# Kernel optimization log

Measured on AMD Instinct MI355X. Metric: run time of the kernel, lower is better.

Reference implementation:

```python
import jax, jax.numpy as jnp
import numpy as np

DIM = 3
N_GRID = 128
DX = 1.0 / N_GRID
INV_DX = float(N_GRID)
DT = 1e-4
P_VOL = (DX * 0.5) ** 2
P_RHO = 1.0
P_MASS = P_VOL * P_RHO
E_MOD = 5000.0
NU = 0.2
MU0 = E_MOD / (2.0 * (1.0 + NU))
LAM0 = E_MOD * NU / ((1.0 + NU) * (1.0 - 2.0 * NU))
N_PARTICLES = 400_000

# 27 stencil offsets of the quadratic B-spline kernel
_OFF = jnp.array([[i, j, k] for i in range(3) for j in range(3) for k in range(3)],
                 dtype=jnp.int32)  # [27,3]


def _substep(x, v, C, F, Jp, gravity, attractor_strength, attractor_pos, material):
    N = x.shape[0]
    dtype = x.dtype
    I3 = jnp.eye(3, dtype=dtype)

    # ---- particle -> grid (P2G) ----
    base = jnp.floor(x * INV_DX - 0.5).astype(jnp.int32)          # [N,3]
    fx = x * INV_DX - base.astype(dtype)                          # [N,3]
    # quadratic kernel weights, w[a, n, d], a in {0,1,2}
    w = jnp.stack([0.5 * (1.5 - fx) ** 2,
                   0.75 - (fx - 1.0) ** 2,
                   0.5 * (fx - 0.5) ** 2], axis=0)                # [3,N,3]

    Fn = jnp.einsum('nij,njk->nik', I3 + DT * C, F)               # deformation update

    h = jnp.clip(jnp.exp(10.0 * (1.0 - Jp)), 0.1, 5.0)
    h = jnp.where(material == 1, 0.3, h)
    mu = jnp.where(material == 0, 0.0, MU0 * h)                   # [N]
    la = LAM0 * h                                                 # [N]

    U, s, Vh = jnp.linalg.svd(Fn, full_matrices=False)            # [N,3,3],[N,3],[N,3,3]

    # faithful to source: plasticity loop only touches first TWO singular values
    J = jnp.ones_like(Jp)
    sig = s
    for d in range(2):
        new_sig = jnp.where(material == 2,
                            jnp.clip(s[:, d], 1.0 - 0.025, 1.0 + 0.0045),
                            s[:, d])
        Jp = Jp * s[:, d] / new_sig
        sig = sig.at[:, d].set(new_sig)
        J = J * new_sig

    F_fluid = jnp.sqrt(J)[:, None, None] * I3                     # material 0
    F_snow = jnpum = None
    F_snow = jnp.einsum('nij,nj,njk->nik', U, sig, Vh)            # material 2: U diag(sig) V^T
    m3 = material[:, None, None]
    Fn = jnp.where(m3 == 0, F_fluid, jnp.where(m3 == 2, F_snow, Fn))

    R = jnp.einsum('nij,njk->nik', U, Vh)                         # U V^T (rotation)
    stress = (2.0 * mu[:, None, None] * jnp.einsum('nij,nkj->nik', Fn - R, Fn)
              + I3 * (la * J * (J - 1.0))[:, None, None])
    stress = (-DT * P_VOL * 4.0 * INV_DX * INV_DX) * stress
    affine = stress + P_MASS * C                                  # [N,3,3]

    # NOTE faithful quirk of the source: weight = w[i][0] * w[j][1] (k-component unused)
    weight = w[_OFF[:, 0], :, 0] * w[_OFF[:, 1], :, 1]            # [27,N]
    dpos = (_OFF[:, None, :].astype(dtype) - fx[None]) * DX       # [27,N,3]
    mom = weight[..., None] * (P_MASS * v[None]
                               + jnp.einsum('nij,onj->oni', affine, dpos))  # [27,N,3]

    idx = base[None] + _OFF[:, None, :]                           # [27,N,3]
    flat = (idx[..., 0] * N_GRID + idx[..., 1]) * N_GRID + idx[..., 2]      # [27,N]
    G3 = N_GRID ** 3
    grid_mom = jnp.zeros((G3, 3), dtype).at[flat.reshape(-1)].add(mom.reshape(-1, 3))
    grid_m = jnp.zeros((G3,), dtype).at[flat.reshape(-1)].add((weight * P_MASS).reshape(-1))

    # ---- grid update ----
    a = jnp.arange(N_GRID, dtype=jnp.int32)
    coords = jnp.stack(jnp.meshgrid(a, a, a, indexing='ij'), axis=-1).reshape(G3, 3)
    mask = grid_m > 0
    m_safe = jnp.where(mask, grid_m, 1.0)
    gv = grid_mom / m_safe[:, None]
    gv = gv + DT * gravity * 30.0
    dist = attractor_pos[None, :] - DX * coords.astype(dtype)
    gv = gv + dist / (0.01 + jnp.linalg.norm(dist, axis=-1, keepdims=True)) \
              * attractor_strength * DT * 100.0
    ic, jc = coords[:, 0], coords[:, 1]
    vx, vy, vz = gv[:, 0], gv[:, 1], gv[:, 2]
    vx = jnp.where((ic < 3) & (vx < 0), 0.0, vx)
    vx = jnp.where((ic > N_GRID - 3) & (vx > 0), 0.0, vx)
    vy = jnp.where((jc < 3) & (vy < 0), 0.0, vy)
    vy = jnp.where((jc > N_GRID - 3) & (vy > 0), 0.0, vy)
    gv = jnp.stack([vx, vy, vz], axis=-1)
    gv = jnp.where(mask[:, None], gv, 0.0)                        # untouched cells stay zero

    # ---- grid -> particle (G2P) ----
    g_v = gv[flat]                                                # [27,N,3]
    dpos2 = _OFF[:, None, :].astype(dtype) - fx[None]             # [27,N,3] (no dx scale)
    new_v = jnp.einsum('on,onc->nc', weight, g_v)                 # [N,3]
    new_C = 4.0 * INV_DX * jnp.einsum('on,onc,ond->ncd', weight, g_v, dpos2)  # [N,3,3]
    x_new = x + DT * new_v

    # pack state: [x(3) | v(3) | Jp(1) | F(9) | C(9)] -> [N,25]
    return jnp.concatenate([x_new, new_v, Jp[:, None],
                            Fn.reshape(N, 9), new_C.reshape(N, 9)], axis=1)


def setup_inputs() -> dict:
    key = jax.random.key(0)
    ks = jax.random.split(key, 9)
    N = N_PARTICLES
    x = 0.1 + 0.8 * jax.random.uniform(ks[0], (N, 3), dtype=jnp.float32)
    v = 0.1 * jax.random.normal(ks[1], (N, 3), dtype=jnp.float32)
    C = 0.01 * jax.random.normal(ks[2], (N, 3, 3), dtype=jnp.float32)
    F = jnp.eye(3, dtype=jnp.float32) + 0.01 * jax.random.normal(ks[3], (N, 3, 3), dtype=jnp.float32)
    Jp = 1.0 + 0.1 * jax.random.uniform(ks[4], (N,), dtype=jnp.float32)
    material = jax.random.randint(ks[5], (N,), 0, 3, dtype=jnp.int32)
    gravity = jnp.array([0.0, -1.0, 0.0], dtype=jnp.float32)
    attractor_strength = jax.random.uniform(ks[6], (), dtype=jnp.float32)
    attractor_pos = jax.random.uniform(ks[7], (3,), dtype=jnp.float32)
    return {"x": x, "v": v, "C": C, "F": F, "Jp": Jp,
            "gravity": gravity, "attractor_strength": attractor_strength,
            "attractor_pos": attractor_pos, "material": material}


def reference(x, v, C, F, Jp, gravity, attractor_strength, attractor_pos, material):
    return _substep(x, v, C, F, Jp, gravity, attractor_strength, attractor_pos, material)
```

## Files before the change

kernel.cpp:

```cpp
#include <hip/hip_runtime.h>

#define NG 128
#define G3 (NG*NG*NG)
#define NSCAN_BLOCKS (G3/256)

__device__ __constant__ const float c_DX      = 1.0f/128.0f;
__device__ __constant__ const float c_INV_DX  = 128.0f;

#define DT      1e-4f
#define P_VOL   ((1.0f/256.0f)*(1.0f/256.0f))
#define P_MASS  P_VOL
#define MU0     (5000.0f/(2.0f*1.2f))
#define LAM0    (5000.0f*0.2f/(1.2f*0.6f))

struct __align__(16) PRec {
    float4 r0, r1, r2, r3;
};

__device__ inline void jacobi_rot(float S[3][3], float V[3][3], int p, int q) {
    float apq = S[p][q];
    if (fabsf(apq) < 1e-24f) return;
    float tau = (S[q][q] - S[p][p]) / (2.0f * apq);
    float t = copysignf(1.0f, tau) / (fabsf(tau) + sqrtf(1.0f + tau*tau));
    float c = rsqrtf(1.0f + t*t);
    float sn = t * c;
    #pragma unroll
    for (int k = 0; k < 3; ++k) {
        float Spk = S[p][k], Sqk = S[q][k];
        S[p][k] = c*Spk - sn*Sqk;
        S[q][k] = sn*Spk + c*Sqk;
    }
    #pragma unroll
    for (int k = 0; k < 3; ++k) {
        float Skp = S[k][p], Skq = S[k][q];
        S[k][p] = c*Skp - sn*Skq;
        S[k][q] = sn*Skp + c*Skq;
    }
    #pragma unroll
    for (int k = 0; k < 3; ++k) {
        float Vkp = V[k][p], Vkq = V[k][q];
        V[k][p] = c*Vkp - sn*Vkq;
        V[k][q] = sn*Vkp + c*Vkq;
    }
}

__device__ inline void svd3(const float A[9], float U[9], float sv[3], float V[9]) {
    float S[3][3];
    #pragma unroll
    for (int i = 0; i < 3; ++i)
        #pragma unroll
        for (int j = 0; j < 3; ++j) {
            float acc = 0.f;
            #pragma unroll
            for (int k = 0; k < 3; ++k) acc += A[k*3+i]*A[k*3+j];
            S[i][j] = acc;
        }
    float Vm[3][3] = {{1.f,0.f,0.f},{0.f,1.f,0.f},{0.f,0.f,1.f}};
    #pragma unroll
    for (int sweep = 0; sweep < 4; ++sweep) {
        jacobi_rot(S, Vm, 0, 1);
        jacobi_rot(S, Vm, 0, 2);
        jacobi_rot(S, Vm, 1, 2);
    }
    float lam[3] = {S[0][0], S[1][1], S[2][2]};
    int i0 = 0, i1 = 1, i2 = 2, t;
    if (lam[i0] < lam[i1]) { t = i0; i0 = i1; i1 = t; }
    if (lam[i0] < lam[i2]) { t = i0; i0 = i2; i2 = t; }
    if (lam[i1] < lam[i2]) { t = i1; i1 = i2; i2 = t; }
    int ord[3] = {i0, i1, i2};
    #pragma unroll
    for (int c = 0; c < 3; ++c) {
        int s_ = ord[c];
        float l = fmaxf(lam[s_], 0.f);
        float sval = sqrtf(l);
        sv[c] = sval;
        float v0 = Vm[0][s_], v1 = Vm[1][s_], v2 = Vm[2][s_];
        V[0*3+c] = v0; V[1*3+c] = v1; V[2*3+c] = v2;
        float inv = (sval > 1e-12f) ? 1.0f/sval : 0.f;
        U[0*3+c] = (A[0]*v0 + A[1]*v1 + A[2]*v2)*inv;
        U[1*3+c] = (A[3]*v0 + A[4]*v1 + A[5]*v2)*inv;
        U[2*3+c] = (A[6]*v0 + A[7]*v1 + A[8]*v2)*inv;
    }
}

__device__ inline void base_from_A(float A0, float A1, float A2,
                                   int& bi, int& bj, int& bk,
                                   float& fx0, float& fx1, float& fx2) {
    float bxf = floorf(A0 - 0.5f);
    float byf = floorf(A1 - 0.5f);
    float bzf = floorf(A2 - 0.5f);
    bi = (int)bxf; bj = (int)byf; bk = (int)bzf;
    bi = min(max(bi, 0), NG-3); bj = min(max(bj, 0), NG-3); bk = min(max(bk, 0), NG-3);
    fx0 = A0 - bxf;
    fx1 = A1 - byf;
    fx2 = A2 - bzf;
}

__global__ void __launch_bounds__(256)
count_kernel(const float* __restrict__ x, int* __restrict__ cell_count, int N) {
    int n = blockIdx.x*256 + threadIdx.x;
    if (n >= N) return;
    int bi, bj, bk; float f0, f1, f2;
    base_from_A(x[3*n+0]*c_INV_DX, x[3*n+1]*c_INV_DX, x[3*n+2]*c_INV_DX,
                bi, bj, bk, f0, f1, f2);
    atomicAdd(&cell_count[(bi*NG + bj)*NG + bk], 1);
}

__global__ void __launch_bounds__(256)
scan_partial_kernel(const int* __restrict__ count, int* __restrict__ partial) {
    __shared__ int red[256];
    int t = threadIdx.x;
    red[t] = count[blockIdx.x*256 + t];
    __syncthreads();
    for (int off = 128; off > 0; off >>= 1) {
        if (t < off) red[t] += red[t+off];
        __syncthreads();
    }
    if (t == 0) partial[blockIdx.x] = red[0];
}

__global__ void __launch_bounds__(256)
scan_partials_kernel(int* __restrict__ partial) {
    __shared__ int part[256];
    int t = threadIdx.x;
    int base = t*32;
    int local[32];
    int s = 0;
    #pragma unroll
    for (int i = 0; i < 32; ++i) { local[i] = s; s += partial[base+i]; }
    part[t] = s;
    __syncthreads();
    for (int off = 1; off < 256; off <<= 1) {
        int v = (t >= off) ? part[t-off] : 0;
        __syncthreads();
        part[t] += v;
        __syncthreads();
    }
    int prev = (t == 0) ? 0 : part[t-1];
    #pragma unroll
    for (int i = 0; i < 32; ++i) partial[base+i] = prev + local[i];
}

__global__ void __launch_bounds__(256)
scan_final_kernel(const int* __restrict__ count, const int* __restrict__ partial,
                  int* __restrict__ offset) {
    __shared__ int part[256];
    int t = threadIdx.x;
    int i = blockIdx.x*256 + t;
    int c = count[i];
    part[t] = c;
    __syncthreads();
    for (int off = 1; off < 256; off <<= 1) {
        int v = (t >= off) ? part[t-off] : 0;
        __syncthreads();
        part[t] += v;
        __syncthreads();
    }
    int base = partial[blockIdx.x];
    offset[i] = base + part[t] - c;
    if (i == G3-1) offset[G3] = base + part[t];
}

__global__ void __launch_bounds__(256)
pre_kernel(const float* __restrict__ x, const float* __restrict__ v,
           const float* __restrict__ Cin, const float* __restrict__ Fin,
           const float* __restrict__ Jp_in, const int* __restrict__ material,
           const int* __restrict__ offset, int* __restrict__ cursor,
           PRec* __restrict__ rec, float* __restrict__ out, int N) {
    int n = blockIdx.x*256 + threadIdx.x;
    if (n >= N) return;

    float A0 = x[3*n+0]*c_INV_DX, A1 = x[3*n+1]*c_INV_DX, A2 = x[3*n+2]*c_INV_DX;
    int bi, bj, bk; float f0, f1, f2;
    base_from_A(A0, A1, A2, bi, bj, bk, f0, f1, f2);

    float Cm[9], Fm[9];
    #pragma unroll
    for (int i = 0; i < 9; ++i) { Cm[i] = Cin[9*n+i]; Fm[i] = Fin[9*n+i]; }

    float Fn[9];
    #pragma unroll
    for (int i = 0; i < 3; ++i)
        #pragma unroll
        for (int k = 0; k < 3; ++k) {
            float acc = Fm[i*3+k];
            #pragma unroll
            for (int j = 0; j < 3; ++j) acc += DT * Cm[i*3+j] * Fm[j*3+k];
            Fn[i*3+k] = acc;
        }

    float Jp = Jp_in[n];
    int mat = material[n];
    float h = expf(10.0f*(1.0f - Jp));
    h = fminf(fmaxf(h, 0.1f), 5.0f);
    if (mat == 1) h = 0.3f;
    float mu = (mat == 0) ? 0.0f : MU0*h;
    float la = LAM0*h;

    float U[9], V[9], sv[3];
    svd3(Fn, U, sv, V);

    float J = 1.0f;
    float sig[3];
    #pragma unroll
    for (int d = 0; d < 2; ++d) {
        float s = sv[d];
        float ns = (mat == 2) ? fminf(fmaxf(s, 1.0f-0.025f), 1.0f+0.0045f) : s;
        Jp = Jp * s / ns;
        sig[d] = ns;
        J *= ns;
    }
    sig[2] = sv[2];

    if (mat == 0) {
        float sj = sqrtf(J);
        Fn[0]=sj; Fn[1]=0; Fn[2]=0; Fn[3]=0; Fn[4]=sj; Fn[5]=0; Fn[6]=0; Fn[7]=0; Fn[8]=sj;
    } else if (mat == 2) {
        #pragma unroll
        for (int i = 0; i < 3; ++i)
            #pragma unroll
            for (int k = 0; k < 3; ++k) {
                float acc = 0.f;
                #pragma unroll
                for (int j = 0; j < 3; ++j) acc += U[i*3+j]*sig[j]*V[k*3+j];
                Fn[i*3+k] = acc;
            }
    }

    float R[9];
    #pragma unroll
    for (int i = 0; i < 3; ++i)
        #pragma unroll
        for (int k = 0; k < 3; ++k) {
            float acc = 0.f;
            #pragma unroll
            for (int j = 0; j < 3; ++j) acc += U[i*3+j]*V[k*3+j];
            R[i*3+k] = acc;
        }

    float press = la * J * (J - 1.0f);
    float scale = -DT * P_VOL * 4.0f * c_INV_DX * c_INV_DX;
    float aff[9];
    #pragma unroll
    for (int i = 0; i < 3; ++i)
        #pragma unroll
        for (int k = 0; k < 3; ++k) {
            float acc = 0.f;
            #pragma unroll
            for (int j = 0; j < 3; ++j) acc += (Fn[i*3+j]-R[i*3+j])*Fn[k*3+j];
            acc = 2.0f*mu*acc;
            if (i == k) acc += press;
            aff[i*3+k] = scale*acc + P_MASS*Cm[i*3+k];
        }

    float* po = out + (size_t)n*25;
    po[6] = Jp;
    #pragma unroll
    for (int i = 0; i < 9; ++i) po[7+i] = Fn[i];

    int cell = (bi*NG + bj)*NG + bk;
    int pos = offset[cell] + atomicAdd(&cursor[cell], 1);

    float4* rp = (float4*)&rec[pos];
    rp[0] = make_float4(A0, A1, A2, __int_as_float(n));
    rp[1] = make_float4(aff[0], aff[1], aff[2], aff[3]);
    rp[2] = make_float4(aff[4], aff[5], aff[6], aff[7]);
    rp[3] = make_float4(aff[8], P_MASS*v[3*n+0], P_MASS*v[3*n+1], P_MASS*v[3*n+2]);
}

__global__ void __launch_bounds__(256)
grid_gather_kernel(const PRec* __restrict__ rec, const int* __restrict__ offset,
                   float4* __restrict__ grid, const float* __restrict__ gravity,
                   const float* __restrict__ attr_s, const float* __restrict__ attr_p) {
    int g2 = blockIdx.x*256 + threadIdx.x;
    int gk2 = g2 & 63;
    int gj  = (g2 >> 6) & (NG-1);
    int gi  = g2 >> 13;
    int zlo = gk2*2, zhi = zlo+1;

    float a0x=0.f, a0y=0.f, a0z=0.f, m0=0.f;
    float a1x=0.f, a1y=0.f, a1z=0.f, m1=0.f;

    int bi0 = max(gi-2, 0), bi1 = min(gi, NG-3);
    int bj0 = max(gj-2, 0), bj1 = min(gj, NG-3);
    int bk0 = max(zlo-2, 0), bk1 = min(zhi, NG-3);

    float gif = (float)gi, gjf = (float)gj, z0f = (float)zlo;

    for (int bi = bi0; bi <= bi1; ++bi) {
        for (int bj = bj0; bj <= bj1; ++bj) {
            int col = (bi*NG + bj)*NG;
            int s = offset[col + bk0];
            int e = offset[col + bk1 + 1];
            for (int p = s; p < e; ++p) {
                const float4* rp = (const float4*)&rec[p];
                float4 r0 = rp[0];
                float4 r1 = rp[1];
                float4 r2 = rp[2];
                float4 r3 = rp[3];

                float ux = gif - r0.x;
                float aux = fabsf(ux);
                float tx = 1.5f - aux;
                float nx = (aux < 0.5f) ? (0.75f - ux*ux) : (0.5f*tx*tx);
                float uy = gjf - r0.y;
                float auy = fabsf(uy);
                float ty = 1.5f - auy;
                float ny = (auy < 0.5f) ? (0.75f - uy*uy) : (0.5f*ty*ty);
                float wgt = nx*ny;

                float uz0 = z0f - r0.z;
                float uz1 = uz0 + 1.0f;
                float w0 = (uz0 > -1.5f && uz0 <= 1.5f) ? wgt : 0.f;
                float w1 = (uz1 > -1.5f && uz1 <= 1.5f) ? wgt : 0.f;

                float dpx = ux*c_DX, dpy = uy*c_DX, dpz0 = uz0*c_DX;
                float sx = r3.y + r1.x*dpx + r1.y*dpy;
                float sy = r3.z + r1.w*dpx + r2.x*dpy;
                float sz = r3.w + r2.z*dpx + r2.w*dpy;
                float c0x = sx + r1.z*dpz0;
                float c0y = sy + r2.y*dpz0;
                float c0z = sz + r3.x*dpz0;
                float c1x = c0x + r1.z*c_DX;
                float c1y = c0y + r2.y*c_DX;
                float c1z = c0z + r3.x*c_DX;
                a0x += w0*c0x; a0y += w0*c0y; a0z += w0*c0z; m0 += w0*P_MASS;
                a1x += w1*c1x; a1y += w1*c1y; a1z += w1*c1z; m1 += w1*P_MASS;
            }
        }
    }

    float gx = DT*gravity[0]*30.0f, gy = DT*gravity[1]*30.0f, gz = DT*gravity[2]*30.0f;
    float apx = attr_p[0], apy = attr_p[1], apz = attr_p[2];
    float as  = attr_s[0] * DT * 100.0f;

    int gidx = (gi*NG + gj)*NG + zlo;
    #pragma unroll
    for (int h = 0; h < 2; ++h) {
        float m   = h ? m1 : m0;
        float mx  = h ? a1x : a0x;
        float my  = h ? a1y : a0y;
        float mz  = h ? a1z : a0z;
        int   gk  = zlo + h;
        float gvx = 0.f, gvy = 0.f, gvz = 0.f;
        if (m > 0.f) {
            float inv = 1.0f/m;
            gvx = mx*inv + gx; gvy = my*inv + gy; gvz = mz*inv + gz;
            float dx_ = apx - c_DX*(float)gi;
            float dy_ = apy - c_DX*(float)gj;
            float dz_ = apz - c_DX*(float)gk;
            float nrm = sqrtf(dx_*dx_ + dy_*dy_ + dz_*dz_);
            float sc = as / (0.01f + nrm);
            gvx += dx_*sc; gvy += dy_*sc; gvz += dz_*sc;
            if (gi < 3      && gvx < 0.f) gvx = 0.f;
            if (gi > NG-3   && gvx > 0.f) gvx = 0.f;
            if (gj < 3      && gvy < 0.f) gvy = 0.f;
            if (gj > NG-3   && gvy > 0.f) gvy = 0.f;
        }
        grid[gidx + h] = make_float4(gvx, gvy, gvz, m);
    }
}

__global__ void __launch_bounds__(256)
g2p_kernel(const PRec* __restrict__ rec, const float4* __restrict__ grid,
           float* __restrict__ out, int N) {
    int gid = blockIdx.x * 256 + threadIdx.x;
    if (gid >= N) return;

    float4 r0 = rec[gid].r0;
    float A0 = r0.x, A1 = r0.y, A2 = r0.z;
    int n = __float_as_int(r0.w);

    int bi, bj, bk; float fx0, fx1, fx2;
    base_from_A(A0, A1, A2, bi, bj, bk, fx0, fx1, fx2);

    float wx[3], wy[3];
    wx[0] = 0.5f*(1.5f-fx0)*(1.5f-fx0); wx[1] = 0.75f-(fx0-1.f)*(fx0-1.f); wx[2] = 0.5f*(fx0-0.5f)*(fx0-0.5f);
    wy[0] = 0.5f*(1.5f-fx1)*(1.5f-fx1); wy[1] = 0.75f-(fx1-1.f)*(fx1-1.f); wy[2] = 0.5f*(fx1-0.5f)*(fx1-0.5f);

    float nvx = 0.f, nvy = 0.f, nvz = 0.f;
    float nC[9];
    #pragma unroll
    for (int i = 0; i < 9; ++i) nC[i] = 0.f;

    #pragma unroll
    for (int i = 0; i < 3; ++i) {
        float dpx = (float)i - fx0;
        #pragma unroll
        for (int j = 0; j < 3; ++j) {
            float wgt = wx[i]*wy[j];
            float dpy = (float)j - fx1;
            int cell0 = ((bi+i)*NG + (bj+j))*NG + bk;
            #pragma unroll
            for (int k = 0; k < 3; ++k) {
                float dpz = (float)k - fx2;
                float4 gv = grid[cell0 + k];
                float wgx = wgt*gv.x, wgy = wgt*gv.y, wgz = wgt*gv.z;
                nvx += wgx; nvy += wgy; nvz += wgz;
                nC[0] += wgx*dpx; nC[1] += wgx*dpy; nC[2] += wgx*dpz;
                nC[3] += wgy*dpx; nC[4] += wgy*dpy; nC[5] += wgy*dpz;
                nC[6] += wgz*dpx; nC[7] += wgz*dpy; nC[8] += wgz*dpz;
            }
        }
    }

    float* po = out + (size_t)n*25;
    float px = A0*c_DX, py = A1*c_DX, pz = A2*c_DX;
    po[0] = px + DT*nvx;
    po[1] = py + DT*nvy;
    po[2] = pz + DT*nvz;
    po[3] = nvx; po[4] = nvy; po[5] = nvz;
    float s4 = 4.0f*c_INV_DX;
    #pragma unroll
    for (int i = 0; i < 9; ++i) po[16+i] = s4*nC[i];
}

extern "C" void kernel_launch(void* const* d_in, const int* in_sizes, int n_in,
                              void* d_out, int out_size, void* d_ws, size_t ws_size,
                              hipStream_t stream) {
    const float* x        = (const float*)d_in[0];
    const float* v        = (const float*)d_in[1];
    const float* C        = (const float*)d_in[2];
    const float* F        = (const float*)d_in[3];
    const float* Jp       = (const float*)d_in[4];
    const float* gravity  = (const float*)d_in[5];
    const float* attr_s   = (const float*)d_in[6];
    const float* attr_p   = (const float*)d_in[7];
    const int*   material = (const int*)d_in[8];
    float* out = (float*)d_out;
    int N = in_sizes[0] / 3;

    char* ws = (char*)d_ws;
    size_t o = 0;
    int* cell_count = (int*)(ws + o);      o += (size_t)G3*sizeof(int);
    int* cursor     = (int*)(ws + o);      o += (size_t)G3*sizeof(int);
    size_t zero_bytes = o;
    int* offset     = (int*)(ws + o);      o += ((size_t)G3+1)*sizeof(int);
    int* partial    = (int*)(ws + o);      o += (size_t)NSCAN_BLOCKS*sizeof(int);
    o = (o + 127) & ~(size_t)127;
    float4* grid    = (float4*)(ws + o);   o += (size_t)G3*sizeof(float4);
    PRec* rec       = (PRec*)(ws + o);     o += (size_t)N*sizeof(PRec);

    hipMemsetAsync(d_ws, 0, zero_bytes, stream);

    int pblocks = (N + 255) / 256;
    count_kernel<<<pblocks, 256, 0, stream>>>(x, cell_count, N);
    scan_partial_kernel<<<NSCAN_BLOCKS, 256, 0, stream>>>(cell_count, partial);
    scan_partials_kernel<<<1, 256, 0, stream>>>(partial);
    scan_final_kernel<<<NSCAN_BLOCKS, 256, 0, stream>>>(cell_count, partial, offset);
    pre_kernel<<<pblocks, 256, 0, stream>>>(x, v, C, F, Jp, material,
                                            offset, cursor, rec, out, N);
    grid_gather_kernel<<<G3/512, 256, 0, stream>>>(rec, offset, grid,
                                                   gravity, attr_s, attr_p);
    g2p_kernel<<<pblocks, 256, 0, stream>>>(rec, grid, out, N);
}
```

Baseline: 296.3 us.

## Gather four z-cells per thread and reuse count-pass atomic ranks for binning

The grid gather kernel now accumulates four consecutive z cells per thread instead of two. Each particle record read from a column is therefore shared across more output cells, and the launch uses half as many blocks. Threads whose stencil range holds no particles now return without writing their grid cells. The count kernel stores each particle's atomic slot index, so the pre kernel no longer needs a second atomic cursor pass or the cursor memset. The trade-off is more accumulator registers per thread and an extra rank buffer of N ints.

```diff
diff --git a/kernel.cpp b/kernel.cpp
--- a/kernel.cpp
+++ b/kernel.cpp
@@ -97,13 +97,14 @@
 }
 
 __global__ void __launch_bounds__(256)
-count_kernel(const float* __restrict__ x, int* __restrict__ cell_count, int N) {
+count_kernel(const float* __restrict__ x, int* __restrict__ cell_count,
+             int* __restrict__ rank, int N) {
     int n = blockIdx.x*256 + threadIdx.x;
     if (n >= N) return;
     int bi, bj, bk; float f0, f1, f2;
     base_from_A(x[3*n+0]*c_INV_DX, x[3*n+1]*c_INV_DX, x[3*n+2]*c_INV_DX,
                 bi, bj, bk, f0, f1, f2);
-    atomicAdd(&cell_count[(bi*NG + bj)*NG + bk], 1);
+    rank[n] = atomicAdd(&cell_count[(bi*NG + bj)*NG + bk], 1);
 }
 
 __global__ void __launch_bounds__(256)
@@ -165,7 +166,7 @@
 pre_kernel(const float* __restrict__ x, const float* __restrict__ v,
            const float* __restrict__ Cin, const float* __restrict__ Fin,
            const float* __restrict__ Jp_in, const int* __restrict__ material,
-           const int* __restrict__ offset, int* __restrict__ cursor,
+           const int* __restrict__ offset, const int* __restrict__ rank,
            PRec* __restrict__ rec, float* __restrict__ out, int N) {
     int n = blockIdx.x*256 + threadIdx.x;
     if (n >= N) return;
@@ -259,7 +260,7 @@
     for (int i = 0; i < 9; ++i) po[7+i] = Fn[i];
 
     int cell = (bi*NG + bj)*NG + bk;
-    int pos = offset[cell] + atomicAdd(&cursor[cell], 1);
+    int pos = offset[cell] + rank[n];
 
     float4* rp = (float4*)&rec[pos];
     rp[0] = make_float4(A0, A1, A2, __int_as_float(n));
@@ -272,26 +273,29 @@
 grid_gather_kernel(const PRec* __restrict__ rec, const int* __restrict__ offset,
                    float4* __restrict__ grid, const float* __restrict__ gravity,
                    const float* __restrict__ attr_s, const float* __restrict__ attr_p) {
-    int g2 = blockIdx.x*256 + threadIdx.x;
-    int gk2 = g2 & 63;
-    int gj  = (g2 >> 6) & (NG-1);
-    int gi  = g2 >> 13;
-    int zlo = gk2*2, zhi = zlo+1;
-
-    float a0x=0.f, a0y=0.f, a0z=0.f, m0=0.f;
-    float a1x=0.f, a1y=0.f, a1z=0.f, m1=0.f;
+    int g4 = blockIdx.x*256 + threadIdx.x;
+    int zq = g4 & 31;
+    int gj = (g4 >> 5) & (NG-1);
+    int gi = g4 >> 12;
+    int zlo = zq*4;
+
+    float ax[4], ay[4], az[4], mm[4];
+    #pragma unroll
+    for (int h = 0; h < 4; ++h) { ax[h]=0.f; ay[h]=0.f; az[h]=0.f; mm[h]=0.f; }
 
     int bi0 = max(gi-2, 0), bi1 = min(gi, NG-3);
     int bj0 = max(gj-2, 0), bj1 = min(gj, NG-3);
-    int bk0 = max(zlo-2, 0), bk1 = min(zhi, NG-3);
+    int bk0 = max(zlo-2, 0), bk1 = min(zlo+3, NG-3);
 
     float gif = (float)gi, gjf = (float)gj, z0f = (float)zlo;
+    bool any = false;
 
     for (int bi = bi0; bi <= bi1; ++bi) {
         for (int bj = bj0; bj <= bj1; ++bj) {
             int col = (bi*NG + bj)*NG;
             int s = offset[col + bk0];
             int e = offset[col + bk1 + 1];
+            if (s < e) any = true;
             for (int p = s; p < e; ++p) {
                 const float4* rp = (const float4*)&rec[p];
                 float4 r0 = rp[0];
@@ -310,25 +314,24 @@
                 float wgt = nx*ny;
 
                 float uz0 = z0f - r0.z;
-                float uz1 = uz0 + 1.0f;
-                float w0 = (uz0 > -1.5f && uz0 <= 1.5f) ? wgt : 0.f;
-                float w1 = (uz1 > -1.5f && uz1 <= 1.5f) ? wgt : 0.f;
-
                 float dpx = ux*c_DX, dpy = uy*c_DX, dpz0 = uz0*c_DX;
-                float sx = r3.y + r1.x*dpx + r1.y*dpy;
-                float sy = r3.z + r1.w*dpx + r2.x*dpy;
-                float sz = r3.w + r2.z*dpx + r2.w*dpy;
-                float c0x = sx + r1.z*dpz0;
-                float c0y = sy + r2.y*dpz0;
-                float c0z = sz + r3.x*dpz0;
-                float c1x = c0x + r1.z*c_DX;
-                float c1y = c0y + r2.y*c_DX;
-                float c1z = c0z + r3.x*c_DX;
-                a0x += w0*c0x; a0y += w0*c0y; a0z += w0*c0z; m0 += w0*P_MASS;
-                a1x += w1*c1x; a1y += w1*c1y; a1z += w1*c1z; m1 += w1*P_MASS;
+                float cx = r3.y + r1.x*dpx + r1.y*dpy + r1.z*dpz0;
+                float cy = r3.z + r1.w*dpx + r2.x*dpy + r2.y*dpz0;
+                float cz = r3.w + r2.z*dpx + r2.w*dpy + r3.x*dpz0;
+                float ix = r1.z*c_DX, iy = r2.y*c_DX, iz = r3.x*c_DX;
+
+                #pragma unroll
+                for (int h = 0; h < 4; ++h) {
+                    float uz = uz0 + (float)h;
+                    float w = (uz > -1.5f && uz <= 1.5f) ? wgt : 0.f;
+                    ax[h] += w*cx; ay[h] += w*cy; az[h] += w*cz; mm[h] += w*P_MASS;
+                    cx += ix; cy += iy; cz += iz;
+                }
             }
         }
     }
+
+    if (!any) return;
 
     float gx = DT*gravity[0]*30.0f, gy = DT*gravity[1]*30.0f, gz = DT*gravity[2]*30.0f;
     float apx = attr_p[0], apy = attr_p[1], apz = attr_p[2];
@@ -336,16 +339,13 @@
 
     int gidx = (gi*NG + gj)*NG + zlo;
     #pragma unroll
-    for (int h = 0; h < 2; ++h) {
-        float m   = h ? m1 : m0;
-        float mx  = h ? a1x : a0x;
-        float my  = h ? a1y : a0y;
-        float mz  = h ? a1z : a0z;
-        int   gk  = zlo + h;
+    for (int h = 0; h < 4; ++h) {
+        float m = mm[h];
+        int gk = zlo + h;
         float gvx = 0.f, gvy = 0.f, gvz = 0.f;
         if (m > 0.f) {
             float inv = 1.0f/m;
-            gvx = mx*inv + gx; gvy = my*inv + gy; gvz = mz*inv + gz;
+            gvx = ax[h]*inv + gx; gvy = ay[h]*inv + gy; gvz = az[h]*inv + gz;
             float dx_ = apx - c_DX*(float)gi;
             float dy_ = apy - c_DX*(float)gj;
             float dz_ = apz - c_DX*(float)gk;
@@ -433,10 +433,10 @@
     char* ws = (char*)d_ws;
     size_t o = 0;
     int* cell_count = (int*)(ws + o);      o += (size_t)G3*sizeof(int);
-    int* cursor     = (int*)(ws + o);      o += (size_t)G3*sizeof(int);
     size_t zero_bytes = o;
     int* offset     = (int*)(ws + o);      o += ((size_t)G3+1)*sizeof(int);
     int* partial    = (int*)(ws + o);      o += (size_t)NSCAN_BLOCKS*sizeof(int);
+    int* rank       = (int*)(ws + o);      o += (size_t)N*sizeof(int);
     o = (o + 127) & ~(size_t)127;
     float4* grid    = (float4*)(ws + o);   o += (size_t)G3*sizeof(float4);
     PRec* rec       = (PRec*)(ws + o);     o += (size_t)N*sizeof(PRec);
@@ -444,13 +444,13 @@
     hipMemsetAsync(d_ws, 0, zero_bytes, stream);
 
     int pblocks = (N + 255) / 256;
-    count_kernel<<<pblocks, 256, 0, stream>>>(x, cell_count, N);
+    count_kernel<<<pblocks, 256, 0, stream>>>(x, cell_count, rank, N);
     scan_partial_kernel<<<NSCAN_BLOCKS, 256, 0, stream>>>(cell_count, partial);
     scan_partials_kernel<<<1, 256, 0, stream>>>(partial);
     scan_final_kernel<<<NSCAN_BLOCKS, 256, 0, stream>>>(cell_count, partial, offset);
     pre_kernel<<<pblocks, 256, 0, stream>>>(x, v, C, F, Jp, material,
-                                            offset, cursor, rec, out, N);
-    grid_gather_kernel<<<G3/512, 256, 0, stream>>>(rec, offset, grid,
-                                                   gravity, attr_s, attr_p);
+                                            offset, rank, rec, out, N);
+    grid_gather_kernel<<<G3/1024, 256, 0, stream>>>(rec, offset, grid,
+                                                    gravity, attr_s, attr_p);
     g2p_kernel<<<pblocks, 256, 0, stream>>>(rec, grid, out, N);
 }
```

Result: faster. 277.5 us (-6.3%).
